# Kernel tuning notes

Hardware: AMD Instinct MI355X
Metric: run time of the kernel (lower is better)

## Reference

```python
import jax, jax.numpy as jnp
import numpy as np

# TT structure: W is [in_features, out_features] = [4096, 4096]
IN_FACTORS = (16, 16, 16)
OUT_FACTORS = (16, 16, 16)
RANKS = (1, 8, 8, 1)
BATCH = 8192
IN_FEATURES = 4096
OUT_FEATURES = 4096
ITER_NUM = 3
L = 1.0
S = -1.0
EPSILON = 1.0


def tt_dense_matmul(cores, mat):
    """Multiply TT-matrix (cores[k]: [r_{k-1}, m_k, n_k, r_k]) by dense mat [prod(n), P].
    Returns [prod(m), P]. Sequential core contractions, never materializes dense W."""
    P = mat.shape[1]
    data = mat.reshape(1, mat.shape[0], P)  # [r=1, N_rem, T]
    M = 1
    for core in cores:
        r0, m, n, r1 = core.shape
        nrem = data.shape[1]
        d4 = data.reshape(r0, n, nrem // n, -1)            # [r0, n_k, N_rem', T]
        data = jnp.einsum('rmns,rnat->satm', core, d4)      # [r1, N_rem', T, m_k]
        data = data.reshape(r1, nrem // n, -1)              # fold m_k into trailing T
        M *= m
    return data.reshape(P, M).T  # [M, P]


def tt_tt_mul(cores_a, cores_b):
    """TT-matrix product: cores of A [M,K] and B [K,N] -> cores of A@B with Kronecker ranks."""
    out = []
    for ca, cb in zip(cores_a, cores_b):
        a0, m, n, a1 = ca.shape
        b0, n2, l, b1 = cb.shape
        c = jnp.einsum('amnb,cnld->acmlbd', ca, cb)
        out.append(c.reshape(a0 * b0, m, l, a1 * b1))
    return out


def setup_inputs() -> dict:
    key = jax.random.key(0)
    ks = jax.random.split(key, 5)
    x = jax.random.normal(ks[0], (BATCH, IN_FEATURES), dtype=jnp.float32)
    # TT cores of weight W [in, out]: core_k shape [r_{k-1}, in_k, out_k, r_k]
    core_std = 0.3  # glorot-like per-core scale
    cores = []
    for k in range(3):
        shp = (RANKS[k], IN_FACTORS[k], OUT_FACTORS[k], RANKS[k + 1])
        cores.append(core_std * jax.random.normal(ks[k + 1], shp, dtype=jnp.float32))
    bias = 0.01 * jnp.ones((OUT_FEATURES,), dtype=jnp.float32)
    return {"x": x, "core0": cores[0], "core1": cores[1], "core2": cores[2], "bias": bias}


def reference(x, core0, core1, core2, bias):
    cores = [core0, core1, core2]
    # weight_t = t3.transpose(weight): swap in/out mode of each core
    cores_t = [c.transpose(0, 2, 1, 3) for c in cores]  # W^T: [out, in]
    x_t = x.T  # [in, B]
    mv = tt_dense_matmul(cores_t, x_t).T  # x @ W, [B, out]
    # norm-gated shrinkage init
    norm_x = jnp.linalg.norm(x)
    x_l = (mv + bias) / L + jnp.where(norm_x > EPSILON, 0.0, S)
    # G = W^T @ W in TT form (ranks grow to 64)
    G = tt_tt_mul(cores_t, cores)
    for _ in range(1, ITER_NUM):
        nrm = jnp.linalg.norm(x_l)
        term = tt_dense_matmul(G, x_l.T).T  # x_l @ (W^T W), [B, out]
        x_l = x_l - term / L + mv / L + bias + jnp.where(nrm > EPSILON, 0.0, S)
    return x_l
```

## Files before the change

kernel.cpp:

```cpp
#include <hip/hip_runtime.h>
#include <stdint.h>

typedef __bf16 bf16;
typedef __bf16 bf16x4 __attribute__((ext_vector_type(4)));
typedef __bf16 bf16x8 __attribute__((ext_vector_type(8)));
typedef float f32x4 __attribute__((ext_vector_type(4)));

#define GLD_LDS16(g, l)                                                        \
  __builtin_amdgcn_global_load_lds(                                            \
      (const __attribute__((address_space(1))) void*)(g),                      \
      (__attribute__((address_space(3))) void*)(l), 16, 0, 0)

#define BAR() asm volatile("s_barrier" ::: "memory")
#define VMW(n) asm volatile("s_waitcnt vmcnt(" #n ")" ::: "memory")
#define PRIO(x) __builtin_amdgcn_s_setprio(x)

__global__ __launch_bounds__(256) void k_pre(
    const float* __restrict__ x, const float* __restrict__ c0,
    const float* __restrict__ c1, const float* __restrict__ c2,
    bf16* __restrict__ Wt, bf16* __restrict__ xb, float* __restrict__ pbuf) {
  const int b = blockIdx.x;
  if (b < 4096) {
    const int j = b;
    const int j0 = j >> 8, j1 = (j >> 4) & 15, j2 = j & 15;
    const int t = threadIdx.x;
    const int i0 = t >> 4, i1 = t & 15;
    float t0[8];
    {
      float4 v0 = *(const float4*)&c0[(i0 * 16 + j0) * 8];
      float4 v1 = *(const float4*)&c0[(i0 * 16 + j0) * 8 + 4];
      t0[0] = v0.x; t0[1] = v0.y; t0[2] = v0.z; t0[3] = v0.w;
      t0[4] = v1.x; t0[5] = v1.y; t0[6] = v1.z; t0[7] = v1.w;
    }
    float a[8];
#pragma unroll
    for (int r2 = 0; r2 < 8; ++r2) a[r2] = 0.f;
#pragma unroll
    for (int r1 = 0; r1 < 8; ++r1) {
      const float* row = &c1[((r1 * 16 + i1) * 16 + j1) * 8];
      float4 u0 = *(const float4*)row;
      float4 u1 = *(const float4*)(row + 4);
      a[0] += t0[r1] * u0.x; a[1] += t0[r1] * u0.y;
      a[2] += t0[r1] * u0.z; a[3] += t0[r1] * u0.w;
      a[4] += t0[r1] * u1.x; a[5] += t0[r1] * u1.y;
      a[6] += t0[r1] * u1.z; a[7] += t0[r1] * u1.w;
    }
    union { bf16 h[16]; bf16x8 v[2]; } u;
#pragma unroll
    for (int i2 = 0; i2 < 16; ++i2) {
      float s = 0.f;
#pragma unroll
      for (int r2 = 0; r2 < 8; ++r2) s += a[r2] * c2[(r2 * 16 + i2) * 16 + j2];
      u.h[i2] = (bf16)s;
    }
    bf16* dst = Wt + (size_t)j * 4096 + i0 * 256 + i1 * 16;
    ((bf16x8*)dst)[0] = u.v[0];
    ((bf16x8*)dst)[1] = u.v[1];
  } else {
    const int n4 = 8192 * 4096 / 4;
    int tid = (b - 4096) * 256 + threadIdx.x;
    const int stride = 1024 * 256;
    const float4* x4 = (const float4*)x;
    bf16x4* xb4 = (bf16x4*)xb;
    float acc = 0.f;
    for (int i = tid; i < n4; i += stride) {
      float4 v = x4[i];
      acc += v.x * v.x + v.y * v.y + v.z * v.z + v.w * v.w;
      bf16x4 bb;
      bb.x = (bf16)v.x; bb.y = (bf16)v.y; bb.z = (bf16)v.z; bb.w = (bf16)v.w;
      xb4[i] = bb;
    }
#pragma unroll
    for (int off = 32; off; off >>= 1) acc += __shfl_down(acc, off);
    __shared__ float red[4];
    if ((threadIdx.x & 63) == 0) red[threadIdx.x >> 6] = acc;
    __syncthreads();
    if (threadIdx.x == 0) pbuf[b - 4096] = red[0] + red[1] + red[2] + red[3];
  }
}

__global__ __launch_bounds__(256) void k_buildG(const float* __restrict__ c0,
                                                const float* __restrict__ c1,
                                                const float* __restrict__ c2,
                                                bf16* __restrict__ G,
                                                const float* __restrict__ pbuf,
                                                float* __restrict__ scal) {
  __shared__ float s_g2[16384];
  __shared__ float s_g0m[16384];
  __shared__ float s_cc[4096];
  const int t = threadIdx.x;
  const int j1 = blockIdx.x >> 4, j1p = blockIdx.x & 15;

  if (blockIdx.x == 0) {
    float a = pbuf[t * 4] + pbuf[t * 4 + 1] + pbuf[t * 4 + 2] + pbuf[t * 4 + 3];
#pragma unroll
    for (int off = 32; off; off >>= 1) a += __shfl_down(a, off);
    if ((t & 63) == 0) s_g2[t >> 6] = a;
    __syncthreads();
    if (t == 0) {
      scal[0] = s_g2[0] + s_g2[1] + s_g2[2] + s_g2[3];
      scal[1] = 0.f; scal[2] = 0.f;
    }
    __syncthreads();
  }

  {
    const float4* c0f = (const float4*)c0;
    const float4* c2f = (const float4*)c2;
    const float4* c1f = (const float4*)c1;
    float4* cc = (float4*)s_cc;
    float4* cm = (float4*)s_g0m;
    for (int k = t; k < 512; k += 256) cc[k] = c0f[k];
    for (int k = t; k < 512; k += 256) cc[512 + k] = c2f[k];
    for (int k = t; k < 4096; k += 256) cm[k] = c1f[k];
  }
  __syncthreads();

  {
    float accg[64];
#pragma unroll
    for (int i = 0; i < 64; ++i) accg[i] = 0.f;
    const int j2 = t >> 4, j2p = t & 15;
    const float* c2L = s_cc + 2048;
#pragma unroll 1
    for (int i2 = 0; i2 < 16; ++i2) {
      float a2[8], b2[8];
#pragma unroll
      for (int r = 0; r < 8; ++r) {
        a2[r] = c2L[(r * 16 + i2) * 16 + j2];
        b2[r] = c2L[(r * 16 + i2) * 16 + j2p];
      }
#pragma unroll
      for (int p2 = 0; p2 < 64; ++p2) accg[p2] += a2[p2 >> 3] * b2[p2 & 7];
    }
#pragma unroll
    for (int p2 = 0; p2 < 64; ++p2) s_g2[p2 * 256 + t] = accg[p2];
  }

  float g0acc[64];
  {
#pragma unroll
    for (int i = 0; i < 64; ++i) g0acc[i] = 0.f;
    const int j0 = t >> 4, j0p = t & 15;
#pragma unroll 1
    for (int i0 = 0; i0 < 16; ++i0) {
      float a0[8], b0[8];
#pragma unroll
      for (int r = 0; r < 8; ++r) {
        a0[r] = s_cc[(i0 * 16 + j0) * 8 + r];
        b0[r] = s_cc[(i0 * 16 + j0p) * 8 + r];
      }
#pragma unroll
      for (int p1 = 0; p1 < 64; ++p1) g0acc[p1] += a0[p1 >> 3] * b0[p1 & 7];
    }
  }
  float g1acc[16];
  {
#pragma unroll
    for (int i = 0; i < 16; ++i) g1acc[i] = 0.f;
    const int p1 = t >> 2, r1 = p1 >> 3, r1p = p1 & 7;
#pragma unroll 1
    for (int i1 = 0; i1 < 16; ++i1) {
      float a1[8], b1[8];
#pragma unroll
      for (int r = 0; r < 8; ++r) {
        a1[r] = s_g0m[((r1 * 16 + i1) * 16 + j1) * 8 + r];
        b1[r] = s_g0m[((r1p * 16 + i1) * 16 + j1p) * 8 + r];
      }
#pragma unroll
      for (int v = 0; v < 16; ++v) {
        int p2 = (t & 3) * 16 + v;
        g1acc[v] += a1[p2 >> 3] * b1[p2 & 7];
      }
    }
  }
  __syncthreads();
#pragma unroll
  for (int p1 = 0; p1 < 64; ++p1) s_g0m[p1 * 256 + t] = g0acc[p1];
#pragma unroll
  for (int v = 0; v < 16; ++v) s_cc[(t >> 2) * 64 + (t & 3) * 16 + v] = g1acc[v];
  __syncthreads();

  float m[64];
#pragma unroll
  for (int i = 0; i < 64; ++i) m[i] = 0.f;
#pragma unroll 4
  for (int p1 = 0; p1 < 64; ++p1) {
    float av = s_g0m[p1 * 256 + t];
#pragma unroll
    for (int q = 0; q < 16; ++q) {
      float4 v = ((const float4*)s_cc)[p1 * 16 + q];
      m[q * 4 + 0] += av * v.x; m[q * 4 + 1] += av * v.y;
      m[q * 4 + 2] += av * v.z; m[q * 4 + 3] += av * v.w;
    }
  }
  __syncthreads();
#pragma unroll
  for (int p2 = 0; p2 < 64; ++p2) s_g0m[p2 * 256 + t] = m[p2];
  __syncthreads();

  const int bcol = (t & 15) * 16;
  const int j2 = t & 15;
#pragma unroll 1
  for (int rep = 0; rep < 2; ++rep) {
    const int r0 = (((t >> 4) + rep * 16)) * 8;
    float acc2[8][16];
#pragma unroll
    for (int i = 0; i < 8; ++i)
#pragma unroll
      for (int c = 0; c < 16; ++c) acc2[i][c] = 0.f;
#pragma unroll 2
    for (int p2 = 0; p2 < 64; ++p2) {
      float4 mv0 = *(const float4*)&s_g0m[p2 * 256 + r0];
      float4 mv1 = *(const float4*)&s_g0m[p2 * 256 + r0 + 4];
      float mv[8] = {mv0.x, mv0.y, mv0.z, mv0.w, mv1.x, mv1.y, mv1.z, mv1.w};
      float gv[16];
#pragma unroll
      for (int q = 0; q < 4; ++q) {
        float4 v = *(const float4*)&s_g2[p2 * 256 + bcol + q * 4];
        gv[q * 4 + 0] = v.x; gv[q * 4 + 1] = v.y;
        gv[q * 4 + 2] = v.z; gv[q * 4 + 3] = v.w;
      }
#pragma unroll
      for (int i = 0; i < 8; ++i)
#pragma unroll
        for (int c = 0; c < 16; ++c) acc2[i][c] += mv[i] * gv[c];
    }
#pragma unroll
    for (int i = 0; i < 8; ++i) {
      const int jj0 = r0 + i;
      const int j0 = jj0 >> 4, j0p = jj0 & 15;
      bf16* d = G + (size_t)(j0 * 256 + j1 * 16 + j2) * 4096 + (j0p * 256 + j1p * 16);
      union { bf16 h[16]; bf16x8 v[2]; } u;
#pragma unroll
      for (int c = 0; c < 16; ++c) u.h[c] = (bf16)acc2[i][c];
      ((bf16x8*)d)[0] = u.v[0];
      ((bf16x8*)d)[1] = u.v[1];
    }
  }
}

#define STAGE_A(h, kt, b)                                                              \
  do {                                                                                 \
    GLD_LDS16(srcA + (size_t)((h) * 128) * K + (kt) * 64,                              \
              smem + (b) * 65536 + (h) * 16384 + wofs);                                \
    GLD_LDS16(srcA + (size_t)((h) * 128 + 64) * K + (kt) * 64,                         \
              smem + (b) * 65536 + (h) * 16384 + 8192 + wofs);                         \
  } while (0)
#define STAGE_B(h, kt, b)                                                              \
  do {                                                                                 \
    GLD_LDS16(srcB + (size_t)((h) * 128) * K + (kt) * 64,                              \
              smem + (b) * 65536 + 32768 + (h) * 16384 + wofs);                        \
    GLD_LDS16(srcB + (size_t)((h) * 128 + 64) * K + (kt) * 64,                         \
              smem + (b) * 65536 + 32768 + (h) * 16384 + 8192 + wofs);                 \
  } while (0)
#define LDA(ms, b)                                                                     \
  do {                                                                                 \
    const char* s_ = smem + (b) * 65536 + (ms) * 16384 + aRow;                         \
    _Pragma("unroll") for (int mi_ = 0; mi_ < 4; ++mi_) {                              \
      af[mi_][0] = *(const bf16x8*)(s_ + mi_ * 2048 + cb0);                            \
      af[mi_][1] = *(const bf16x8*)(s_ + mi_ * 2048 + cb1);                            \
    }                                                                                  \
  } while (0)
#define LDB(ns, b)                                                                     \
  do {                                                                                 \
    const char* s_ = smem + (b) * 65536 + 32768 + (ns) * 16384 + bRow;                 \
    _Pragma("unroll") for (int ni_ = 0; ni_ < 2; ++ni_) {                              \
      bfr[ns][ni_][0] = *(const bf16x8*)(s_ + ni_ * 2048 + cb0);                       \
      bfr[ns][ni_][1] = *(const bf16x8*)(s_ + ni_ * 2048 + cb1);                       \
    }                                                                                  \
  } while (0)
#define MQ(ms, ns)                                                                     \
  do {                                                                                 \
    PRIO(1);                                                                           \
    _Pragma("unroll") for (int mi_ = 0; mi_ < 4; ++mi_)                                \
    _Pragma("unroll") for (int ni_ = 0; ni_ < 2; ++ni_)                                \
    _Pragma("unroll") for (int ks_ = 0; ks_ < 2; ++ks_)                                \
        acc[(ms) * 4 + mi_][(ns) * 2 + ni_] =                                          \
            __builtin_amdgcn_mfma_f32_16x16x32_bf16(                                   \
                af[mi_][ks_], bfr[ns][ni_][ks_],                                       \
                acc[(ms) * 4 + mi_][(ns) * 2 + ni_], 0, 0, 0);                         \
    PRIO(0);                                                                           \
  } while (0)

__device__ __forceinline__ void run_core(const bf16* __restrict__ Ag,
                                         const bf16* __restrict__ Bg, const int K,
                                         const int bx, const int by, char* smem,
                                         f32x4 (&acc)[8][4]) {
  const int t = threadIdx.x;
  const int w = t >> 6, lane = t & 63;
  const int q = lane >> 4, lr = lane & 15;
  const int wm = w & 1, wn = w >> 1;

  const int r0 = t >> 3;
  const int ksrc = (t & 7) ^ (r0 & 7);
  const bf16* srcA = Ag + (size_t)(by * 256 + r0) * K + ksrc * 8;
  const bf16* srcB = Bg + (size_t)(bx * 256 + r0) * K + ksrc * 8;
  const int wofs = w << 10;

  const int aRow = (wm * 64 + lr) * 128;
  const int bRow = (wn * 32 + lr) * 128;
  const int cb0 = ((q ^ (lr & 7)) << 4);
  const int cb1 = (((4 + q) ^ (lr & 7)) << 4);

#pragma unroll
  for (int i = 0; i < 8; ++i)
#pragma unroll
    for (int j = 0; j < 4; ++j) acc[i][j] = (f32x4){0.f, 0.f, 0.f, 0.f};

  bf16x8 af[4][2];
  bf16x8 bfr[2][2][2];

  STAGE_A(0, 0, 0); STAGE_B(0, 0, 0); STAGE_B(1, 0, 0); STAGE_A(1, 0, 0);
  STAGE_A(0, 1, 1); STAGE_B(0, 1, 1); STAGE_B(1, 1, 1);
  VMW(6);
  BAR();

  const int NT = K >> 6;
#pragma unroll 1
  for (int tt = 0; tt + 3 < NT; tt += 2) {
    STAGE_A(1, tt + 1, 1);
    LDB(0, 0); LDA(0, 0); LDB(1, 0);
    MQ(0, 0); MQ(0, 1);
    BAR();
    STAGE_A(0, tt + 2, 0); STAGE_B(0, tt + 2, 0); STAGE_B(1, tt + 2, 0);
    LDA(1, 0);
    MQ(1, 1); MQ(1, 0);
    VMW(6);
    BAR();
    STAGE_A(1, tt + 2, 0);
    LDB(0, 1); LDA(0, 1); LDB(1, 1);
    MQ(0, 0); MQ(0, 1);
    BAR();
    STAGE_A(0, tt + 3, 1); STAGE_B(0, tt + 3, 1); STAGE_B(1, tt + 3, 1);
    LDA(1, 1);
    MQ(1, 1); MQ(1, 0);
    VMW(6);
    BAR();
  }

  STAGE_A(1, NT - 1, 1);
  LDB(0, 0); LDA(0, 0); LDB(1, 0);
  MQ(0, 0); MQ(0, 1);
  BAR();
  LDA(1, 0);
  MQ(1, 1); MQ(1, 0);
  VMW(0);
  BAR();
  LDB(0, 1); LDA(0, 1); LDB(1, 1);
  MQ(0, 0); MQ(0, 1);
  BAR();
  LDA(1, 1);
  MQ(1, 1); MQ(1, 0);
}

template <int MODE>
__global__ __launch_bounds__(512, 2) void k_gemm(
    const bf16* __restrict__ A, const bf16* __restrict__ Bt, int M, int N, int K,
    const float* __restrict__ bias, const bf16* __restrict__ xl0,
    const bf16* __restrict__ xl_prev, float* f32_out, bf16* __restrict__ bf_out,
    const float* __restrict__ ssq_a, const float* __restrict__ ssq_b,
    float* __restrict__ ssq_out) {
  const int nb = gridDim.x * gridDim.y;
  const int lin = blockIdx.y * gridDim.x + blockIdx.x;
  const int sw = (lin & 7) * (nb >> 3) + (lin >> 3);
  const int bx = sw % gridDim.x, by = sw / gridDim.x;
  __shared__ char smem[131072];

  float gate = 0.f;
  if constexpr (MODE == 0) {
    gate = (*ssq_a > 1.0f) ? 0.f : -1.f;
  } else {
    float g0v = (*ssq_a > 1.0f) ? 0.f : -1.f;
    float gtv = (*ssq_b > 1.0f) ? 0.f : -1.f;
    gate = gtv - g0v;
  }
  VMW(0);

  f32x4 acc[8][4];
  run_core(A, Bt, K, bx, by, smem, acc);

  const int t = threadIdx.x;
  const int w = t >> 6, lane = t & 63;
  const int q = lane >> 4, lr = lane & 15;
  const int wm = w & 1, wn = w >> 1;
  float ssql = 0.f;
#pragma unroll
  for (int mi = 0; mi < 8; ++mi) {
    const int grow = by * 256 + ((mi & 4) ? 128 : 0) + wm * 64 + (mi & 3) * 16 + q * 4;
#pragma unroll
    for (int r = 0; r < 4; ++r) {
      const size_t rowb = (size_t)(grow + r) * N;
#pragma unroll
      for (int ni = 0; ni < 4; ++ni) {
        const int gcol = bx * 256 + ((ni & 2) ? 128 : 0) + wn * 32 + (ni & 1) * 16 + lr;
        const size_t idx = rowb + gcol;
        float v = acc[mi][ni][r];
        if constexpr (MODE == 0) {
          float xl = v + bias[gcol] + gate;
          bf_out[idx] = (bf16)xl;
          ssql += xl * xl;
        } else if constexpr (MODE == 2) {
          float xl = 2.0f * (float)xl0[idx] - v + gate;
          bf_out[idx] = (bf16)xl;
          ssql += xl * xl;
        } else {
          f32_out[idx] = (float)xl_prev[idx] - v + (float)xl0[idx] + gate;
        }
      }
    }
  }
  if constexpr (MODE == 0 || MODE == 2) {
#pragma unroll
    for (int off = 32; off; off >>= 1) ssql += __shfl_down(ssql, off);
    __syncthreads();
    float* red = (float*)smem;
    if (lane == 0) red[w] = ssql;
    __syncthreads();
    if (t == 0) {
      float s = 0.f;
#pragma unroll
      for (int i = 0; i < 8; ++i) s += red[i];
      atomicAdd(ssq_out, s);
    }
  }
}

extern "C" void kernel_launch(void* const* d_in, const int* in_sizes, int n_in,
                              void* d_out, int out_size, void* d_ws, size_t ws_size,
                              hipStream_t stream) {
  const float* x = (const float*)d_in[0];
  const float* c0 = (const float*)d_in[1];
  const float* c1 = (const float*)d_in[2];
  const float* c2 = (const float*)d_in[3];
  const float* bias = (const float*)d_in[4];
  float* out = (float*)d_out;

  const int B = 8192, F = 4096;
  char* ws = (char*)d_ws;
  float* scal = (float*)ws;
  bf16* xbf = (bf16*)(ws + 256);
  bf16* Wt = (bf16*)(ws + 256 + (size_t)67108864);
  bf16* G = (bf16*)(ws + 256 + (size_t)100663296);
  bf16* xl0 = (bf16*)(ws + 256 + (size_t)134217728);
  bf16* xl1 = xbf;
  float* pbuf = (float*)xl0;

  k_pre<<<5120, 256, 0, stream>>>(x, c0, c1, c2, Wt, xbf, pbuf);
  k_buildG<<<256, 256, 0, stream>>>(c0, c1, c2, G, pbuf, scal);

  dim3 g1d(F / 256, B / 256);
  k_gemm<0><<<g1d, 512, 0, stream>>>(xbf, Wt, B, F, F, bias, nullptr, nullptr,
                                     nullptr, xl0, &scal[0], nullptr, &scal[1]);
  k_gemm<2><<<g1d, 512, 0, stream>>>(xl0, G, B, F, F, nullptr, xl0, nullptr,
                                     nullptr, xl1, &scal[0], &scal[1], &scal[2]);
  k_gemm<3><<<g1d, 512, 0, stream>>>(xl1, G, B, F, F, nullptr, xl0, xl1,
                                     out, nullptr, &scal[0], &scal[2], nullptr);
}
```

Before: 993.7 us.

## Retile GEMM to 128x256 blocks with 256 threads and 3-stage K=32 pipeline

The dense GEMM kernels move from a 256x256 tile with 512 threads and a double-buffered K=64 stage to a 128x256 tile with 256 threads and a triple-buffered K=32 stage. Each wave now computes a 64x128 subtile using 4x8 MFMAs per stage, with a new XOR swizzle matched to the 64-byte LDS rows. The LDS footprint drops from 128 KB to 72 KB, which may let more blocks share a CU and deepens prefetch. The cost is lower arithmetic intensity per block, more barriers per unit of K, and higher register pressure from 32 accumulators per thread.

Measured after the change: 1.118 ms. 12.5% more time.

```diff
diff --git a/kernel.cpp b/kernel.cpp
--- a/kernel.cpp
+++ b/kernel.cpp
@@ -240,122 +240,96 @@
   }
 }
 
-#define STAGE_A(h, kt, b)                                                              \
+#define STAGE(kt, b)                                                                   \
   do {                                                                                 \
-    GLD_LDS16(srcA + (size_t)((h) * 128) * K + (kt) * 64,                              \
-              smem + (b) * 65536 + (h) * 16384 + wofs);                                \
-    GLD_LDS16(srcA + (size_t)((h) * 128 + 64) * K + (kt) * 64,                         \
-              smem + (b) * 65536 + (h) * 16384 + 8192 + wofs);                         \
+    GLD_LDS16(srcA + (size_t)(kt) * 32, smem + (b) * 24576 + wofs);                    \
+    GLD_LDS16(srcA + (size_t)64 * K + (kt) * 32, smem + (b) * 24576 + 4096 + wofs);    \
+    GLD_LDS16(srcB + (size_t)(kt) * 32, smem + (b) * 24576 + 8192 + wofs);             \
+    GLD_LDS16(srcB + (size_t)64 * K + (kt) * 32,                                       \
+              smem + (b) * 24576 + 12288 + wofs);                                      \
+    GLD_LDS16(srcB + (size_t)128 * K + (kt) * 32,                                      \
+              smem + (b) * 24576 + 16384 + wofs);                                      \
+    GLD_LDS16(srcB + (size_t)192 * K + (kt) * 32,                                      \
+              smem + (b) * 24576 + 20480 + wofs);                                      \
   } while (0)
-#define STAGE_B(h, kt, b)                                                              \
+#define LDF(b)                                                                         \
   do {                                                                                 \
-    GLD_LDS16(srcB + (size_t)((h) * 128) * K + (kt) * 64,                              \
-              smem + (b) * 65536 + 32768 + (h) * 16384 + wofs);                        \
-    GLD_LDS16(srcB + (size_t)((h) * 128 + 64) * K + (kt) * 64,                         \
-              smem + (b) * 65536 + 32768 + (h) * 16384 + 8192 + wofs);                 \
+    const char* As_ = smem + (b) * 24576;                                              \
+    const char* Bs_ = smem + (b) * 24576 + 8192;                                       \
+    _Pragma("unroll") for (int mi_ = 0; mi_ < 4; ++mi_)                                \
+        af[mi_] = *(const bf16x8*)(As_ + (wm * 64 + mi_ * 16 + lr) * 64 + cb);         \
+    _Pragma("unroll") for (int ni_ = 0; ni_ < 8; ++ni_)                                \
+        bfr[ni_] = *(const bf16x8*)(Bs_ + (wn * 128 + ni_ * 16 + lr) * 64 + cb);       \
   } while (0)
-#define LDA(ms, b)                                                                     \
-  do {                                                                                 \
-    const char* s_ = smem + (b) * 65536 + (ms) * 16384 + aRow;                         \
-    _Pragma("unroll") for (int mi_ = 0; mi_ < 4; ++mi_) {                              \
-      af[mi_][0] = *(const bf16x8*)(s_ + mi_ * 2048 + cb0);                            \
-      af[mi_][1] = *(const bf16x8*)(s_ + mi_ * 2048 + cb1);                            \
-    }                                                                                  \
-  } while (0)
-#define LDB(ns, b)                                                                     \
-  do {                                                                                 \
-    const char* s_ = smem + (b) * 65536 + 32768 + (ns) * 16384 + bRow;                 \
-    _Pragma("unroll") for (int ni_ = 0; ni_ < 2; ++ni_) {                              \
-      bfr[ns][ni_][0] = *(const bf16x8*)(s_ + ni_ * 2048 + cb0);                       \
-      bfr[ns][ni_][1] = *(const bf16x8*)(s_ + ni_ * 2048 + cb1);                       \
-    }                                                                                  \
-  } while (0)
-#define MQ(ms, ns)                                                                     \
+#define MQ_ALL()                                                                       \
   do {                                                                                 \
     PRIO(1);                                                                           \
     _Pragma("unroll") for (int mi_ = 0; mi_ < 4; ++mi_)                                \
-    _Pragma("unroll") for (int ni_ = 0; ni_ < 2; ++ni_)                                \
-    _Pragma("unroll") for (int ks_ = 0; ks_ < 2; ++ks_)                                \
-        acc[(ms) * 4 + mi_][(ns) * 2 + ni_] =                                          \
-            __builtin_amdgcn_mfma_f32_16x16x32_bf16(                                   \
-                af[mi_][ks_], bfr[ns][ni_][ks_],                                       \
-                acc[(ms) * 4 + mi_][(ns) * 2 + ni_], 0, 0, 0);                         \
+    _Pragma("unroll") for (int ni_ = 0; ni_ < 8; ++ni_)                                \
+        acc[mi_][ni_] = __builtin_amdgcn_mfma_f32_16x16x32_bf16(                       \
+            af[mi_], bfr[ni_], acc[mi_][ni_], 0, 0, 0);                                \
     PRIO(0);                                                                           \
   } while (0)
 
 __device__ __forceinline__ void run_core(const bf16* __restrict__ Ag,
                                          const bf16* __restrict__ Bg, const int K,
                                          const int bx, const int by, char* smem,
-                                         f32x4 (&acc)[8][4]) {
+                                         f32x4 (&acc)[4][8]) {
   const int t = threadIdx.x;
   const int w = t >> 6, lane = t & 63;
   const int q = lane >> 4, lr = lane & 15;
   const int wm = w & 1, wn = w >> 1;
 
-  const int r0 = t >> 3;
-  const int ksrc = (t & 7) ^ (r0 & 7);
-  const bf16* srcA = Ag + (size_t)(by * 256 + r0) * K + ksrc * 8;
-  const bf16* srcB = Bg + (size_t)(bx * 256 + r0) * K + ksrc * 8;
+  const int r0 = t >> 2;
+  const int colc = ((t & 3) ^ ((r0 >> 1) & 3)) * 8;
+  const bf16* srcA = Ag + (size_t)(by * 128 + r0) * K + colc;
+  const bf16* srcB = Bg + (size_t)(bx * 256 + r0) * K + colc;
   const int wofs = w << 10;
 
-  const int aRow = (wm * 64 + lr) * 128;
-  const int bRow = (wn * 32 + lr) * 128;
-  const int cb0 = ((q ^ (lr & 7)) << 4);
-  const int cb1 = (((4 + q) ^ (lr & 7)) << 4);
-
-#pragma unroll
-  for (int i = 0; i < 8; ++i)
-#pragma unroll
-    for (int j = 0; j < 4; ++j) acc[i][j] = (f32x4){0.f, 0.f, 0.f, 0.f};
-
-  bf16x8 af[4][2];
-  bf16x8 bfr[2][2][2];
-
-  STAGE_A(0, 0, 0); STAGE_B(0, 0, 0); STAGE_B(1, 0, 0); STAGE_A(1, 0, 0);
-  STAGE_A(0, 1, 1); STAGE_B(0, 1, 1); STAGE_B(1, 1, 1);
+  const int cb = (q ^ ((lr >> 1) & 3)) << 4;
+
+#pragma unroll
+  for (int i = 0; i < 4; ++i)
+#pragma unroll
+    for (int j = 0; j < 8; ++j) acc[i][j] = (f32x4){0.f, 0.f, 0.f, 0.f};
+
+  bf16x8 af[4];
+  bf16x8 bfr[8];
+
+  STAGE(0, 0);
+  STAGE(1, 1);
   VMW(6);
   BAR();
 
-  const int NT = K >> 6;
+  const int NT = K >> 5;
 #pragma unroll 1
-  for (int tt = 0; tt + 3 < NT; tt += 2) {
-    STAGE_A(1, tt + 1, 1);
-    LDB(0, 0); LDA(0, 0); LDB(1, 0);
-    MQ(0, 0); MQ(0, 1);
-    BAR();
-    STAGE_A(0, tt + 2, 0); STAGE_B(0, tt + 2, 0); STAGE_B(1, tt + 2, 0);
-    LDA(1, 0);
-    MQ(1, 1); MQ(1, 0);
+  for (int tt = 0; tt < NT - 2; tt += 3) {
+    STAGE(tt + 2, 2);
+    LDF(0);
+    MQ_ALL();
     VMW(6);
     BAR();
-    STAGE_A(1, tt + 2, 0);
-    LDB(0, 1); LDA(0, 1); LDB(1, 1);
-    MQ(0, 0); MQ(0, 1);
-    BAR();
-    STAGE_A(0, tt + 3, 1); STAGE_B(0, tt + 3, 1); STAGE_B(1, tt + 3, 1);
-    LDA(1, 1);
-    MQ(1, 1); MQ(1, 0);
+    STAGE(tt + 3, 0);
+    LDF(1);
+    MQ_ALL();
     VMW(6);
     BAR();
-  }
-
-  STAGE_A(1, NT - 1, 1);
-  LDB(0, 0); LDA(0, 0); LDB(1, 0);
-  MQ(0, 0); MQ(0, 1);
-  BAR();
-  LDA(1, 0);
-  MQ(1, 1); MQ(1, 0);
+    STAGE(tt + 4, 1);
+    LDF(2);
+    MQ_ALL();
+    VMW(6);
+    BAR();
+  }
+  LDF(0);
+  MQ_ALL();
   VMW(0);
   BAR();
-  LDB(0, 1); LDA(0, 1); LDB(1, 1);
-  MQ(0, 0); MQ(0, 1);
-  BAR();
-  LDA(1, 1);
-  MQ(1, 1); MQ(1, 0);
+  LDF(1);
+  MQ_ALL();
 }
 
 template <int MODE>
-__global__ __launch_bounds__(512, 2) void k_gemm(
+__global__ __launch_bounds__(256, 2) void k_gemm(
     const bf16* __restrict__ A, const bf16* __restrict__ Bt, int M, int N, int K,
     const float* __restrict__ bias, const bf16* __restrict__ xl0,
     const bf16* __restrict__ xl_prev, float* f32_out, bf16* __restrict__ bf_out,
@@ -365,7 +339,7 @@
   const int lin = blockIdx.y * gridDim.x + blockIdx.x;
   const int sw = (lin & 7) * (nb >> 3) + (lin >> 3);
   const int bx = sw % gridDim.x, by = sw / gridDim.x;
-  __shared__ char smem[131072];
+  __shared__ char smem[73728];
 
   float gate = 0.f;
   if constexpr (MODE == 0) {
@@ -377,7 +351,7 @@
   }
   VMW(0);
 
-  f32x4 acc[8][4];
+  f32x4 acc[4][8];
   run_core(A, Bt, K, bx, by, smem, acc);
 
   const int t = threadIdx.x;
@@ -386,14 +360,14 @@
   const int wm = w & 1, wn = w >> 1;
   float ssql = 0.f;
 #pragma unroll
-  for (int mi = 0; mi < 8; ++mi) {
-    const int grow = by * 256 + ((mi & 4) ? 128 : 0) + wm * 64 + (mi & 3) * 16 + q * 4;
+  for (int mi = 0; mi < 4; ++mi) {
+    const int grow = by * 128 + wm * 64 + mi * 16 + q * 4;
 #pragma unroll
     for (int r = 0; r < 4; ++r) {
       const size_t rowb = (size_t)(grow + r) * N;
 #pragma unroll
-      for (int ni = 0; ni < 4; ++ni) {
-        const int gcol = bx * 256 + ((ni & 2) ? 128 : 0) + wn * 32 + (ni & 1) * 16 + lr;
+      for (int ni = 0; ni < 8; ++ni) {
+        const int gcol = bx * 256 + wn * 128 + ni * 16 + lr;
         const size_t idx = rowb + gcol;
         float v = acc[mi][ni][r];
         if constexpr (MODE == 0) {
@@ -417,12 +391,7 @@
     float* red = (float*)smem;
     if (lane == 0) red[w] = ssql;
     __syncthreads();
-    if (t == 0) {
-      float s = 0.f;
-#pragma unroll
-      for (int i = 0; i < 8; ++i) s += red[i];
-      atomicAdd(ssq_out, s);
-    }
+    if (t == 0) atomicAdd(ssq_out, red[0] + red[1] + red[2] + red[3]);
   }
 }
 
@@ -449,11 +418,11 @@
   k_pre<<<5120, 256, 0, stream>>>(x, c0, c1, c2, Wt, xbf, pbuf);
   k_buildG<<<256, 256, 0, stream>>>(c0, c1, c2, G, pbuf, scal);
 
-  dim3 g1d(F / 256, B / 256);
-  k_gemm<0><<<g1d, 512, 0, stream>>>(xbf, Wt, B, F, F, bias, nullptr, nullptr,
+  dim3 g1d(F / 256, B / 128);
+  k_gemm<0><<<g1d, 256, 0, stream>>>(xbf, Wt, B, F, F, bias, nullptr, nullptr,
                                      nullptr, xl0, &scal[0], nullptr, &scal[1]);
-  k_gemm<2><<<g1d, 512, 0, stream>>>(xl0, G, B, F, F, nullptr, xl0, nullptr,
+  k_gemm<2><<<g1d, 256, 0, stream>>>(xl0, G, B, F, F, nullptr, xl0, nullptr,
                                      nullptr, xl1, &scal[0], &scal[1], &scal[2]);
-  k_gemm<3><<<g1d, 512, 0, stream>>>(xl1, G, B, F, F, nullptr, xl0, xl1,
+  k_gemm<3><<<g1d, 256, 0, stream>>>(xl1, G, B, F, F, nullptr, xl0, xl1,
                                      out, nullptr, &scal[0], &scal[2], nullptr);
 }
```
